# Performance work log

Measured on AMD Instinct MI355X. Metric: run time of the kernel, lower is better.

## Reference

```python
import jax, jax.numpy as jnp
import numpy as np

B, N = 16384, 20
F = 128          # n_node_features = n_neighbors_features = embed_dim
T = 100          # time_dim
E = 128          # n_edge_features
H = 2            # n_head
OUT = 128        # output_dimension
KEY_DIM = F + T + E  # 356


def setup_inputs() -> dict:
    key = jax.random.key(0)
    ks = jax.random.split(key, 24)
    s = 0.02
    inp = {
        "src_node_features": jax.random.normal(ks[0], (B, F), jnp.float32),
        "neighbors_features": jax.random.normal(ks[1], (B, N, F), jnp.float32),
        "neighbors_time_features": jax.random.normal(ks[2], (B, N, T), jnp.float32),
        "edge_features": jax.random.normal(ks[3], (B, N, E), jnp.float32),
        "neighbors_padding_mask": jax.random.randint(ks[4], (B, N), 0, 2).astype(bool),
        "weights": jax.random.uniform(ks[5], (B, N), jnp.float32),
        # transform: Linear(key_dim -> F)
        "Wt": jax.random.normal(ks[6], (F, KEY_DIM), jnp.float32) * s,
        "bt": jnp.zeros((F,), jnp.float32),
        # MultiheadAttention projections (embed_dim = kdim = vdim = F)
        "Wq": jax.random.normal(ks[7], (F, F), jnp.float32) * s,
        "bq": jnp.zeros((F,), jnp.float32),
        "Wk": jax.random.normal(ks[8], (F, F), jnp.float32) * s,
        "bk": jnp.zeros((F,), jnp.float32),
        "Wv": jax.random.normal(ks[9], (F, F), jnp.float32) * s,
        "bv": jnp.zeros((F,), jnp.float32),
        "Wo": jax.random.normal(ks[10], (F, F), jnp.float32) * s,
        "bo": jnp.zeros((F,), jnp.float32),
        # MergeLayer: fc1(query_dim + F -> F), fc2(F -> OUT)
        "W1": jax.random.normal(ks[11], (F, F + F), jnp.float32) * s,
        "b1": jnp.zeros((F,), jnp.float32),
        "W2": jax.random.normal(ks[12], (OUT, F), jnp.float32) * s,
        "b2": jnp.zeros((OUT,), jnp.float32),
    }
    return inp


def _gat_forward(src, nbr, timef, edgef, w, mask,
                 Wt, bt, Wq, bq, Wk, bk, Wv, bv, Wo, bo, W1, b1, W2, b2):
    b, f = src.shape
    dh = f // H
    scale = 1.0 / jnp.sqrt(jnp.asarray(dh, src.dtype))
    # key = transform(cat([nbr, edge, time])) * weights  -> [B,N,F]
    k_in = jnp.concatenate([nbr, edgef, timef], axis=2)
    keyv = (jnp.einsum('bnk,fk->bnf', k_in, Wt) + bt) * w[:, :, None]
    # invalid-neighborhood fixup: rows fully padded get their first slot unmasked
    invalid = mask.all(axis=1, keepdims=True)           # [B,1]
    mask = mask.at[:, 0].set(jnp.where(invalid[:, 0], False, mask[:, 0]))
    # projections (query_len = 1)
    q = (src @ Wq.T + bq).reshape(b, H, dh)             # [B,H,dh]
    k = (keyv @ Wk.T + bk).reshape(b, N, H, dh)         # [B,N,H,dh]
    v = (keyv @ Wv.T + bv).reshape(b, N, H, dh)
    scores = jnp.einsum('bhd,bnhd->bhn', q, k) * scale  # [B,H,N]
    scores = jnp.where(mask[:, None, :], -jnp.inf, scores)
    attn = jax.nn.softmax(scores, axis=-1)
    ctx = jnp.einsum('bhn,bnhd->bhd', attn, v).reshape(b, f)
    out = ctx @ Wo.T + bo                               # [B,F]
    out = jnp.where(invalid, jnp.asarray(0.0, out.dtype), out)
    out = jax.nn.relu(out)
    # MergeLayer: fc2(relu(fc1(cat([attn_out, src]))))
    hmid = jax.nn.relu(jnp.concatenate([out, src], axis=1) @ W1.T + b1)
    return hmid @ W2.T + b2


def reference(src_node_features, neighbors_features, neighbors_time_features,
              edge_features, neighbors_padding_mask, weights,
              Wt, bt, Wq, bq, Wk, bk, Wv, bv, Wo, bo, W1, b1, W2, b2):
    return _gat_forward(src_node_features, neighbors_features,
                        neighbors_time_features, edge_features, weights,
                        neighbors_padding_mask,
                        Wt, bt, Wq, bq, Wk, bk, Wv, bv, Wo, bo, W1, b1, W2, b2)
```

## Files before the change

kernel.cpp:

```cpp
#include <hip/hip_runtime.h>
#include <math.h>

#define NN 20
#define FF 128
#define TT 100
#define EE 128
#define KD 356

typedef unsigned int u32;
typedef unsigned short u16;
typedef unsigned long long u64;
typedef __attribute__((ext_vector_type(4))) float f32x4;
typedef __attribute__((ext_vector_type(8))) short s16x8;

__device__ __forceinline__ u16 f2b(float f) {
    u32 u = __float_as_uint(f);
    u32 r = u + 0x7FFFu + ((u >> 16) & 1u);
    return (u16)(r >> 16);
}
__device__ __forceinline__ float b2f(u16 h) { return __uint_as_float(((u32)h) << 16); }
__device__ __forceinline__ float blo(u32 u){ return __uint_as_float(u << 16); }
__device__ __forceinline__ float bhi(u32 u){ return __uint_as_float(u & 0xFFFF0000u); }
__device__ __forceinline__ u32 pk2(float a, float b){ return (u32)f2b(a) | ((u32)f2b(b) << 16); }


__global__ void prep_fuse(const float* __restrict__ Wt, const float* __restrict__ bt,
                          const float* __restrict__ Wk, const float* __restrict__ Wv,
                          const u32* __restrict__ maskw,
                          float* __restrict__ wkt, float* __restrict__ wvt,
                          float* __restrict__ kfb, float* __restrict__ vfb, int* __restrict__ flagp)
{
    const int blk = blockIdx.x, t = threadIdx.x;
    if (blk < KD) {
        __shared__ float col[FF];
        col[t] = Wt[t * KD + blk];
        __syncthreads();
        float ak = 0.f, av = 0.f;
        for (int j = 0; j < FF; ++j) {
            float c = col[j];
            ak = fmaf(Wk[t * FF + j], c, ak);
            av = fmaf(Wv[t * FF + j], c, av);
        }
        wkt[blk * FF + t] = ak;
        wvt[blk * FF + t] = av;
    } else if (blk == KD) {
        float ak = 0.f, av = 0.f;
        for (int j = 0; j < FF; ++j) {
            float c = bt[j];
            ak = fmaf(Wk[t * FF + j], c, ak);
            av = fmaf(Wv[t * FF + j], c, av);
        }
        kfb[t] = ak; vfb[t] = av;
    } else {
        int any = 0;
        for (int i = t; i < 8192; i += 128) any |= (maskw[i] > 1u) ? 1 : 0;
        any = __any(any) ? 1 : 0;
        __shared__ int red[2];
        if ((t & 63) == 0) red[t >> 6] = any;
        __syncthreads();
        if (t == 0) *flagp = (red[0] | red[1]) ? 1 : 0;
    }
}

__global__ void prep_pack_v3(const float* __restrict__ wkt, const float* __restrict__ wvt,
                             const float* __restrict__ Wq, const float* __restrict__ Wo,
                             const float* __restrict__ W1, const float* __restrict__ W2,
                             u16* __restrict__ kvB, u16* __restrict__ wqI, u16* __restrict__ woI,
                             u16* __restrict__ w1I, u16* __restrict__ w2I)
{
    const int id = blockIdx.x * 256 + threadIdx.x;
    if (id < 122880) {
        int kt = id / 10240, rem = id % 10240;
        int n = rem / 40, kk = rem % 40;
        int k = kt * 32 + kk;
        float v = 0.f;
        if (kk < 32 && k < KD) v = (n < FF) ? wkt[k * FF + n] : wvt[k * FF + (n - FF)];
        kvB[id] = f2b(v);
    } else if (id < 141312) {
        int e = id - 122880; int rem = e % 9216;
        int n = rem / 72, kk = rem % 72; int k = (e / 9216) * 64 + kk;
        wqI[e] = f2b(kk < 64 ? Wq[n * FF + k] : 0.f);
    } else if (id < 159744) {
        int e = id - 141312; int rem = e % 9216;
        int n = rem / 72, kk = rem % 72; int k = (e / 9216) * 64 + kk;
        woI[e] = f2b(kk < 64 ? Wo[n * FF + k] : 0.f);
    } else if (id < 196608) {
        int e = id - 159744; int rem = e % 9216;
        int n = rem / 72, kk = rem % 72; int k = (e / 9216) * 64 + kk;
        w1I[e] = f2b(kk < 64 ? W1[n * 2 * FF + k] : 0.f);
    } else if (id < 215040) {
        int e = id - 196608; int rem = e % 9216;
        int n = rem / 72, kk = rem % 72; int k = (e / 9216) * 64 + kk;
        w2I[e] = f2b(kk < 64 ? W2[n * FF + k] : 0.f);
    }
}

__device__ __forceinline__ void load_a_tile(const float* __restrict__ nbr,
                                            const float* __restrict__ edg,
                                            const float* __restrict__ tmf,
                                            size_t r, int cg, int kt, f32x4& v0, f32x4& v1)
{
    int c0 = cg * 8;
    if (kt < 4) {
        const float* p = nbr + r * 128 + kt * 32 + c0;
        v0 = *(const f32x4*)p; v1 = *(const f32x4*)(p + 4);
    } else if (kt < 8) {
        const float* p = edg + r * 128 + (kt - 4) * 32 + c0;
        v0 = *(const f32x4*)p; v1 = *(const f32x4*)(p + 4);
    } else {
        int c = (kt - 8) * 32 + c0;
        const float* p = tmf + r * 100 + c;
        v0 = (c + 3 < 100) ? *(const f32x4*)p : (f32x4){0.f,0.f,0.f,0.f};
        v1 = (c + 7 < 100) ? *(const f32x4*)(p + 4) : (f32x4){0.f,0.f,0.f,0.f};
    }
}

__global__ __launch_bounds__(512) void kv_gemm_v3(
    const float* __restrict__ nbr, const float* __restrict__ edg, const float* __restrict__ tmf,
    const float* __restrict__ wgt, const float* __restrict__ bk, const float* __restrict__ bv,
    const u16* __restrict__ kvB, const float* __restrict__ kfb, const float* __restrict__ vfb,
    u16* __restrict__ kvout)
{
    __shared__ u16 lA[128 * 40];
    __shared__ u16 lB[256 * 40];
    const int tid = threadIdx.x;
    const int Mbase = blockIdx.x * 128;
    const int lane = tid & 63, wave = tid >> 6;
    const int wm = wave >> 2, wn = wave & 3;
    const int row = tid >> 2;
    const int cg  = tid & 3;

    f32x4 acc[4][4] = {};
    const size_t r = (size_t)(Mbase + row);

    f32x4 v0, v1;
    load_a_tile(nbr, edg, tmf, r, cg, 0, v0, v1);

    for (int kt = 0; kt < 12; ++kt) {
        u32 p0 = pk2(v0.x, v0.y), p1 = pk2(v0.z, v0.w);
        u32 p2 = pk2(v1.x, v1.y), p3 = pk2(v1.z, v1.w);
        __syncthreads();
        *(uint4*)(&lA[row * 40 + cg * 8]) = make_uint4(p0, p1, p2, p3);
        for (int c = wave; c < 20; c += 8) {
            const char* g = (const char*)kvB + (size_t)kt * 20480 + c * 1024 + lane * 16;
            char* l = (char*)lB + c * 1024;
            __builtin_amdgcn_global_load_lds((const __attribute__((address_space(1))) u32*)g,
                                             (__attribute__((address_space(3))) u32*)l, 16, 0, 0);
        }
        if (kt < 11) load_a_tile(nbr, edg, tmf, r, cg, kt + 1, v0, v1);
        __syncthreads();

        const int kkb = (lane >> 4) * 8;
        s16x8 a[4], b[4];
        #pragma unroll
        for (int mt = 0; mt < 4; ++mt) {
            int m = wm * 64 + mt * 16 + (lane & 15);
            a[mt] = *(const s16x8*)(&lA[m * 40 + kkb]);
        }
        #pragma unroll
        for (int nt = 0; nt < 4; ++nt) {
            int n = wn * 64 + nt * 16 + (lane & 15);
            b[nt] = *(const s16x8*)(&lB[n * 40 + kkb]);
        }
        #pragma unroll
        for (int mt = 0; mt < 4; ++mt)
            #pragma unroll
            for (int nt = 0; nt < 4; ++nt)
                acc[mt][nt] = __builtin_amdgcn_mfma_f32_16x16x32_bf16(a[mt], b[nt], acc[mt][nt], 0, 0, 0);
    }

    #pragma unroll
    for (int mt = 0; mt < 4; ++mt) {
        float w4[4];
        #pragma unroll
        for (int i = 0; i < 4; ++i)
            w4[i] = wgt[Mbase + wm * 64 + mt * 16 + (lane >> 4) * 4 + i];
        #pragma unroll
        for (int nt = 0; nt < 4; ++nt) {
            int c = wn * 64 + nt * 16 + (lane & 15);
            float fb   = (c < FF) ? kfb[c] : vfb[c - FF];
            float bias = (c < FF) ? bk[c]  : bv[c - FF];
            #pragma unroll
            for (int i = 0; i < 4; ++i) {
                int rr = Mbase + wm * 64 + mt * 16 + (lane >> 4) * 4 + i;
                float val = fmaf(acc[mt][nt][i] + fb, w4[i], bias);
                kvout[(size_t)rr * 256 + c] = f2b(val);
            }
        }
    }
}

__global__ __launch_bounds__(64) void attn_lite(
    const u16* __restrict__ kv, const u16* __restrict__ Q, const void* __restrict__ maskp,
    const int* __restrict__ flagp, u16* __restrict__ ctx, unsigned char* __restrict__ flags)
{
    const int b = blockIdx.x, t = threadIdx.x;
    __shared__ u32 kls[NN][69];
    __shared__ float s_q[FF];
    __shared__ float s_sc[2 * NN];

    const int flag = *flagp;
    bool mybit = false;
    if (t < NN) {
        if (flag) mybit = ((const unsigned char*)maskp)[b * NN + t] != 0;
        else      mybit = ((const int*)maskp)[b * NN + t] != 0;
    }
    u64 bal = __ballot(mybit);
    u32 mb = (u32)(bal & 0xFFFFFull);
    const bool invalid = (mb == 0xFFFFFu);
    if (invalid) mb &= ~1u;
    if (t == 0) flags[b] = invalid ? 1 : 0;

    u32 qw = ((const u32*)Q)[(size_t)b * 64 + t];
    s_q[2 * t] = blo(qw); s_q[2 * t + 1] = bhi(qw);

    u32 vw[NN];
    const u32* kvp = (const u32*)kv + (size_t)b * NN * 128;
    #pragma unroll
    for (int n = 0; n < NN; ++n) {
        kls[n][t] = kvp[n * 128 + t];
        vw[n] = kvp[n * 128 + 64 + t];
    }
    __syncthreads();

    if (t < 2 * NN) {
        int h = t / NN, n = t - (t / NN) * NN;
        const u32* kr = &kls[n][h * 32];
        const float* qr = s_q + h * 64;
        float s = 0.f;
        #pragma unroll
        for (int d = 0; d < 32; ++d) {
            u32 u = kr[d];
            s = fmaf(qr[2 * d],     blo(u), s);
            s = fmaf(qr[2 * d + 1], bhi(u), s);
        }
        s *= 0.125f;
        s_sc[t] = ((mb >> n) & 1u) ? -INFINITY : s;
    }
    __syncthreads();
    if (t < 2) {
        float mx = -INFINITY;
        for (int n = 0; n < NN; ++n) mx = fmaxf(mx, s_sc[t * NN + n]);
        float e[NN]; float sum = 0.f;
        for (int n = 0; n < NN; ++n) { e[n] = expf(s_sc[t * NN + n] - mx); sum += e[n]; }
        float inv = 1.f / sum;
        for (int n = 0; n < NN; ++n) s_sc[t * NN + n] = e[n] * inv;
    }
    __syncthreads();

    const int h = t >> 5;
    float c0 = 0.f, c1 = 0.f;
    #pragma unroll
    for (int n = 0; n < NN; ++n) {
        float p = s_sc[h * NN + n];
        c0 = fmaf(p, blo(vw[n]), c0);
        c1 = fmaf(p, bhi(vw[n]), c1);
    }
    ((u32*)ctx)[(size_t)b * 64 + t] = pk2(c0, c1);
}

#define GM_Q 0
#define GM_O 1
#define GM_H 2
#define GM_F 3

template<int MODE>
__global__ __launch_bounds__(256) void gemm_small(
    const void* __restrict__ Asrc, const float* __restrict__ Asrc2,
    const u16* __restrict__ Bimg, const float* __restrict__ bias,
    const unsigned char* __restrict__ flags, void* __restrict__ outp)
{
    __shared__ u16 lA[64 * 72];
    __shared__ u16 lB[128 * 72];
    const int tid = threadIdx.x;
    const int Mbase = blockIdx.x * 64;
    const int lane = tid & 63, wave = tid >> 6;
    const int wm = wave >> 1, wn = wave & 1;
    const int row = tid >> 2, cg = tid & 3;

    constexpr int KTILES = (MODE == GM_H) ? 4 : 2;
    f32x4 acc[2][4] = {};
    const size_t r = (size_t)(Mbase + row);

    for (int kt = 0; kt < KTILES; ++kt) {
        if (MODE == GM_Q || (MODE == GM_H && kt >= 2)) {
            const float* ap = (MODE == GM_Q)
                ? ((const float*)Asrc + r * 128 + kt * 64 + cg * 16)
                : (Asrc2 + r * 128 + (kt - 2) * 64 + cg * 16);
            f32x4 x0 = *(const f32x4*)ap,       x1 = *(const f32x4*)(ap + 4);
            f32x4 x2 = *(const f32x4*)(ap + 8), x3 = *(const f32x4*)(ap + 12);
            *(uint4*)(&lA[row * 72 + cg * 16])     = make_uint4(pk2(x0.x,x0.y), pk2(x0.z,x0.w), pk2(x1.x,x1.y), pk2(x1.z,x1.w));
            *(uint4*)(&lA[row * 72 + cg * 16 + 8]) = make_uint4(pk2(x2.x,x2.y), pk2(x2.z,x2.w), pk2(x3.x,x3.y), pk2(x3.z,x3.w));
        } else {
            const u16* ap = (const u16*)Asrc + r * 128 + kt * 64 + cg * 16;
            *(uint4*)(&lA[row * 72 + cg * 16])     = *(const uint4*)ap;
            *(uint4*)(&lA[row * 72 + cg * 16 + 8]) = *(const uint4*)(ap + 8);
        }
        for (int c = wave; c < 18; c += 4) {
            const char* g = (const char*)Bimg + (size_t)kt * 18432 + c * 1024 + lane * 16;
            char* l = (char*)lB + c * 1024;
            __builtin_amdgcn_global_load_lds((const __attribute__((address_space(1))) u32*)g,
                                             (__attribute__((address_space(3))) u32*)l, 16, 0, 0);
        }
        __syncthreads();
        #pragma unroll
        for (int ks = 0; ks < 2; ++ks) {
            int kk = ks * 32 + (lane >> 4) * 8;
            s16x8 a[2], b[4];
            #pragma unroll
            for (int mt = 0; mt < 2; ++mt)
                a[mt] = *(const s16x8*)(&lA[(wm * 32 + mt * 16 + (lane & 15)) * 72 + kk]);
            #pragma unroll
            for (int nt = 0; nt < 4; ++nt)
                b[nt] = *(const s16x8*)(&lB[(wn * 64 + nt * 16 + (lane & 15)) * 72 + kk]);
            #pragma unroll
            for (int mt = 0; mt < 2; ++mt)
                #pragma unroll
                for (int nt = 0; nt < 4; ++nt)
                    acc[mt][nt] = __builtin_amdgcn_mfma_f32_16x16x32_bf16(a[mt], b[nt], acc[mt][nt], 0, 0, 0);
        }
        __syncthreads();
    }

    #pragma unroll
    for (int mt = 0; mt < 2; ++mt) {
        #pragma unroll
        for (int nt = 0; nt < 4; ++nt) {
            int colg = wn * 64 + nt * 16 + (lane & 15);
            float bb = bias[colg];
            #pragma unroll
            for (int i = 0; i < 4; ++i) {
                int rg = Mbase + wm * 32 + mt * 16 + (lane >> 4) * 4 + i;
                float val = acc[mt][nt][i] + bb;
                if (MODE == GM_O) { if (flags[rg]) val = 0.f; val = fmaxf(val, 0.f); }
                if (MODE == GM_H) val = fmaxf(val, 0.f);
                if (MODE == GM_F) ((float*)outp)[(size_t)rg * 128 + colg] = val;
                else              ((u16*)outp)[(size_t)rg * 128 + colg] = f2b(val);
            }
        }
    }
}


__global__ void prep_pack_r2(const float* __restrict__ wkt, const float* __restrict__ wvt,
                             const float* __restrict__ Wq, const float* __restrict__ Wo,
                             const float* __restrict__ W1, const float* __restrict__ W2,
                             u16* __restrict__ bpack, u32* __restrict__ wq2, u32* __restrict__ wo2,
                             u32* __restrict__ w12, u32* __restrict__ w22)
{
    const int id = blockIdx.x * 256 + threadIdx.x;
    if (id < 98304) {
        int kt = id >> 14;
        int o  = id & 16383;
        int n  = o >> 6;
        int kk = (o & 63) ^ ((n & 7) << 3);
        int k  = kt * 64 + kk;
        float v = 0.f;
        if (k < KD) v = (n < FF) ? wkt[k * FF + n] : wvt[k * FF + (n - FF)];
        bpack[id] = f2b(v);
    } else if (id < 106496) {
        int e = id - 98304; int j = e >> 6, tt = e & 63;
        wq2[e] = (u32)f2b(Wq[tt * FF + j]) | ((u32)f2b(Wq[(tt + 64) * FF + j]) << 16);
    } else if (id < 114688) {
        int e = id - 106496; int j = e >> 6, tt = e & 63;
        wo2[e] = (u32)f2b(Wo[tt * FF + j]) | ((u32)f2b(Wo[(tt + 64) * FF + j]) << 16);
    } else if (id < 131072) {
        int e = id - 114688; int j = e >> 6, tt = e & 63;
        w12[e] = (u32)f2b(W1[tt * 2 * FF + j]) | ((u32)f2b(W1[(tt + 64) * 2 * FF + j]) << 16);
    } else if (id < 139264) {
        int e = id - 131072; int j = e >> 6, tt = e & 63;
        w22[e] = (u32)f2b(W2[tt * FF + j]) | ((u32)f2b(W2[(tt + 64) * FF + j]) << 16);
    }
}

__global__ __launch_bounds__(512) void kv_gemm_r2(
    const float* __restrict__ nbr, const float* __restrict__ edg, const float* __restrict__ tmf,
    const float* __restrict__ wgt, const float* __restrict__ bk, const float* __restrict__ bv,
    const u16* __restrict__ bpack, const float* __restrict__ kfb, const float* __restrict__ vfb,
    u16* __restrict__ kvout)
{
    __shared__ u16 lA[128 * 64];
    __shared__ u16 lB[256 * 64];
    const int tid = threadIdx.x;
    const int Mbase = blockIdx.x * 128;
    const int lane = tid & 63, wave = tid >> 6;
    const int wm = wave >> 2, wn = wave & 3;

    f32x4 acc[4][4] = {};
    const int rq = tid >> 4;
    const int cq = tid & 15;

    for (int kt = 0; kt < 6; ++kt) {
        #pragma unroll
        for (int i = 0; i < 4; ++i) {
            int row = rq + i * 32;
            size_t r = (size_t)(Mbase + row);
            f32x4 v;
            if (kt < 2)       v = *(const f32x4*)(nbr + r * 128 + kt * 64 + cq * 4);
            else if (kt < 4)  v = *(const f32x4*)(edg + r * 128 + (kt - 2) * 64 + cq * 4);
            else if (kt == 4) v = *(const f32x4*)(tmf + r * 100 + cq * 4);
            else if (cq < 9)  v = *(const f32x4*)(tmf + r * 100 + 64 + cq * 4);
            else              v = (f32x4){0.f, 0.f, 0.f, 0.f};
            int off = row * 64 + ((cq * 4) ^ ((row & 7) << 3));
            *(uint2*)(&lA[off]) = make_uint2(pk2(v.x, v.y), pk2(v.z, v.w));
        }
        #pragma unroll
        for (int i = 0; i < 4; ++i) {
            int boff = wave * 4096 + i * 1024;
            const char* g = (const char*)bpack + (size_t)kt * 32768 + boff + lane * 16;
            char* l = (char*)lB + boff;
            __builtin_amdgcn_global_load_lds((const __attribute__((address_space(1))) u32*)g,
                                             (__attribute__((address_space(3))) u32*)l, 16, 0, 0);
        }
        __syncthreads();
        #pragma unroll
        for (int ks = 0; ks < 2; ++ks) {
            int kk = ks * 32 + (lane >> 4) * 8;
            s16x8 a[4], b[4];
            #pragma unroll
            for (int mt = 0; mt < 4; ++mt) {
                int m = wm * 64 + mt * 16 + (lane & 15);
                a[mt] = *(const s16x8*)(&lA[m * 64 + (kk ^ ((m & 7) << 3))]);
            }
            #pragma unroll
            for (int nt = 0; nt < 4; ++nt) {
                int n = wn * 64 + nt * 16 + (lane & 15);
                b[nt] = *(const s16x8*)(&lB[n * 64 + (kk ^ ((n & 7) << 3))]);
            }
            #pragma unroll
            for (int mt = 0; mt < 4; ++mt)
                #pragma unroll
                for (int nt = 0; nt < 4; ++nt)
                    acc[mt][nt] = __builtin_amdgcn_mfma_f32_16x16x32_bf16(a[mt], b[nt], acc[mt][nt], 0, 0, 0);
        }
        __syncthreads();
    }

    #pragma unroll
    for (int mt = 0; mt < 4; ++mt) {
        float w4[4];
        #pragma unroll
        for (int i = 0; i < 4; ++i)
            w4[i] = wgt[Mbase + wm * 64 + mt * 16 + (lane >> 4) * 4 + i];
        #pragma unroll
        for (int nt = 0; nt < 4; ++nt) {
            int c = wn * 64 + nt * 16 + (lane & 15);
            float fb   = (c < FF) ? kfb[c] : vfb[c - FF];
            float bias = (c < FF) ? bk[c]  : bv[c - FF];
            #pragma unroll
            for (int i = 0; i < 4; ++i) {
                int rr = Mbase + wm * 64 + mt * 16 + (lane >> 4) * 4 + i;
                float val = fmaf(acc[mt][nt][i] + fb, w4[i], bias);
                kvout[(size_t)rr * 256 + c] = f2b(val);
            }
        }
    }
}

__global__ __launch_bounds__(64) void gat_attn_r2(
    const float* __restrict__ src, const void* __restrict__ maskp,
    const float* __restrict__ bq, const float* __restrict__ bo,
    const float* __restrict__ b1, const float* __restrict__ b2,
    const u16* __restrict__ kv, const u32* __restrict__ wq2, const u32* __restrict__ wo2,
    const u32* __restrict__ w12, const u32* __restrict__ w22,
    const int* __restrict__ flagp, float* __restrict__ out)
{
    const int b = blockIdx.x, t = threadIdx.x;
    __shared__ u16 kls[NN * 132];
    __shared__ float s_src[FF], s_q[FF], s_ctx[FF], s_out[FF], s_h[FF];
    __shared__ float s_sc[2 * NN];

    const int flag = *flagp;
    bool mybit = false;
    if (t < NN) {
        if (flag) mybit = ((const unsigned char*)maskp)[b * NN + t] != 0;
        else      mybit = ((const int*)maskp)[b * NN + t] != 0;
    }
    u64 bal = __ballot(mybit);
    u32 mb = (u32)(bal & 0xFFFFFull);
    const bool invalid = (mb == 0xFFFFFu);
    if (invalid) mb &= ~1u;

    s_src[t] = src[(size_t)b * FF + t];
    s_src[t + 64] = src[(size_t)b * FF + 64 + t];

    float v0[NN], v1[NN];
    #pragma unroll
    for (int n = 0; n < NN; ++n) {
        const u16* row = kv + ((size_t)b * NN + n) * 256;
        kls[n * 132 + t]      = row[t];
        kls[n * 132 + 64 + t] = row[64 + t];
        v0[n] = b2f(row[128 + t]);
        v1[n] = b2f(row[192 + t]);
    }
    __syncthreads();

    {
        float q0 = bq[t], q1 = bq[64 + t];
        for (int j = 0; j < FF; ++j) {
            u32 u = wq2[j * 64 + t];
            float sj = s_src[j];
            q0 = fmaf(blo(u), sj, q0);
            q1 = fmaf(bhi(u), sj, q1);
        }
        s_q[t] = q0; s_q[64 + t] = q1;
    }
    __syncthreads();

    if (t < 2 * NN) {
        int h = t / NN, n = t - (t / NN) * NN;
        const u16* kr = kls + n * 132 + h * 64;
        const float* qr = s_q + h * 64;
        float s = 0.f;
        #pragma unroll
        for (int d = 0; d < 64; ++d) s = fmaf(qr[d], b2f(kr[d]), s);
        s *= 0.125f;
        s_sc[t] = ((mb >> n) & 1u) ? -INFINITY : s;
    }
    __syncthreads();
    if (t < 2) {
        float mx = -INFINITY;
        for (int n = 0; n < NN; ++n) mx = fmaxf(mx, s_sc[t * NN + n]);
        float e[NN]; float sum = 0.f;
        for (int n = 0; n < NN; ++n) { e[n] = expf(s_sc[t * NN + n] - mx); sum += e[n]; }
        float inv = 1.f / sum;
        for (int n = 0; n < NN; ++n) s_sc[t * NN + n] = e[n] * inv;
    }
    __syncthreads();

    {
        float c0 = 0.f, c1 = 0.f;
        #pragma unroll
        for (int n = 0; n < NN; ++n) {
            c0 = fmaf(s_sc[n],      v0[n], c0);
            c1 = fmaf(s_sc[NN + n], v1[n], c1);
        }
        s_ctx[t] = c0; s_ctx[64 + t] = c1;
    }
    __syncthreads();

    {
        float o0 = bo[t], o1 = bo[64 + t];
        for (int j = 0; j < FF; ++j) {
            u32 u = wo2[j * 64 + t];
            float cj = s_ctx[j];
            o0 = fmaf(blo(u), cj, o0);
            o1 = fmaf(bhi(u), cj, o1);
        }
        if (invalid) { o0 = 0.f; o1 = 0.f; }
        o0 = fmaxf(o0, 0.f); o1 = fmaxf(o1, 0.f);
        s_out[t] = o0; s_out[64 + t] = o1;
    }
    __syncthreads();

    {
        float h0 = b1[t], h1 = b1[64 + t];
        for (int j = 0; j < FF; ++j) {
            u32 u = w12[j * 64 + t];
            float xj = s_out[j];
            h0 = fmaf(blo(u), xj, h0);
            h1 = fmaf(bhi(u), xj, h1);
        }
        for (int j = 0; j < FF; ++j) {
            u32 u = w12[(FF + j) * 64 + t];
            float xj = s_src[j];
            h0 = fmaf(blo(u), xj, h0);
            h1 = fmaf(bhi(u), xj, h1);
        }
        h0 = fmaxf(h0, 0.f); h1 = fmaxf(h1, 0.f);
        s_h[t] = h0; s_h[64 + t] = h1;
    }
    __syncthreads();

    {
        float f0 = b2[t], f1 = b2[64 + t];
        for (int j = 0; j < FF; ++j) {
            u32 u = w22[j * 64 + t];
            float hj = s_h[j];
            f0 = fmaf(blo(u), hj, f0);
            f1 = fmaf(bhi(u), hj, f1);
        }
        out[(size_t)b * FF + t] = f0;
        out[(size_t)b * FF + 64 + t] = f1;
    }
}


#define FB_WKT  0
#define FB_WVT  (FB_WKT + KD*FF)
#define FB_KB   (FB_WVT + KD*FF)
#define FB_VB   (FB_KB + FF)
#define FB_WQT  (FB_VB + FF)
#define FB_WOT  (FB_WQT + FF*FF)
#define FB_W1T  (FB_WOT + FF*FF)
#define FB_W2T  (FB_W1T + 2*FF*FF)
#define FB_FLAG (FB_W2T + FF*FF)

__global__ void gat_prep_fb(const float* __restrict__ Wt, const float* __restrict__ bt,
                            const float* __restrict__ Wq, const float* __restrict__ Wk,
                            const float* __restrict__ Wv, const float* __restrict__ Wo,
                            const float* __restrict__ W1, const float* __restrict__ W2,
                            const u32* __restrict__ maskw, float* __restrict__ ws)
{
    const int blk = blockIdx.x;
    const int t = threadIdx.x;
    if (blk < KD) {
        __shared__ float col[FF];
        col[t] = Wt[t * KD + blk];
        __syncthreads();
        float ak = 0.f, av = 0.f;
        for (int j = 0; j < FF; ++j) {
            float c = col[j];
            ak = fmaf(Wk[t * FF + j], c, ak);
            av = fmaf(Wv[t * FF + j], c, av);
        }
        ws[FB_WKT + blk * FF + t] = ak;
        ws[FB_WVT + blk * FF + t] = av;
    } else if (blk == KD) {
        float ak = 0.f, av = 0.f;
        for (int j = 0; j < FF; ++j) {
            float c = bt[j];
            ak = fmaf(Wk[t * FF + j], c, ak);
            av = fmaf(Wv[t * FF + j], c, av);
        }
        ws[FB_KB + t] = ak;
        ws[FB_VB + t] = av;
    } else if (blk == KD + 1) {
        int any = 0;
        for (int i = t; i < 8192; i += 128) any |= (maskw[i] > 1u) ? 1 : 0;
        any = __any(any) ? 1 : 0;
        __shared__ int red[2];
        if ((t & 63) == 0) red[t >> 6] = any;
        __syncthreads();
        if (t == 0) ((int*)ws)[FB_FLAG] = (red[0] | red[1]) ? 1 : 0;
    } else {
        int id = (blk - (KD + 2)) * 128 + t;
        if (id < FF * FF) {
            int k = id >> 7, f = id & 127;
            ws[FB_WQT + id] = Wq[f * FF + k];
        } else if (id < 2 * FF * FF) {
            int e = id - FF * FF; int k = e >> 7, f = e & 127;
            ws[FB_WOT + e] = Wo[f * FF + k];
        } else if (id < 4 * FF * FF) {
            int e = id - 2 * FF * FF; int j = e >> 7, f = e & 127;
            ws[FB_W1T + e] = W1[f * (2 * FF) + j];
        } else if (id < 5 * FF * FF) {
            int e = id - 4 * FF * FF; int k = e >> 7, f = e & 127;
            ws[FB_W2T + e] = W2[f * FF + k];
        }
    }
}

__global__ __launch_bounds__(64) void gat_main_fb(
    const float* __restrict__ src, const float* __restrict__ nbr,
    const float* __restrict__ tmf, const float* __restrict__ edg,
    const void* __restrict__ maskp, const float* __restrict__ wgt,
    const float* __restrict__ bq, const float* __restrict__ bk,
    const float* __restrict__ bv, const float* __restrict__ bo,
    const float* __restrict__ b1, const float* __restrict__ b2,
    const float* __restrict__ ws, float* __restrict__ out)
{
    const int b = blockIdx.x;
    const int t = threadIdx.x;
    __shared__ __align__(16) float kin[KD * NN];
    __shared__ float s_src[FF], s_q[FF], s_ctx[FF], s_out[FF], s_h[FF];
    __shared__ float s_w[NN], s_sc[2 * NN];

    const int flag = ((const int*)ws)[FB_FLAG];
    bool mybit = false;
    if (t < NN) {
        if (flag) mybit = ((const unsigned char*)maskp)[b * NN + t] != 0;
        else      mybit = ((const int*)maskp)[b * NN + t] != 0;
    }
    u64 bal = __ballot(mybit);
    u32 mb = (u32)(bal & 0xFFFFFull);
    const bool invalid = (mb == 0xFFFFFu);
    if (invalid) mb &= ~1u;

    s_src[t] = src[(size_t)b * FF + t];
    s_src[t + 64] = src[(size_t)b * FF + 64 + t];
    if (t < NN) s_w[t] = wgt[(size_t)b * NN + t];

    for (int idx = t; idx < NN * FF; idx += 64) {
        int n = idx >> 7, j = idx & 127;
        kin[j * NN + n]         = nbr[((size_t)b * NN + n) * FF + j];
        kin[(128 + j) * NN + n] = edg[((size_t)b * NN + n) * EE + j];
    }
    for (int idx = t; idx < NN * TT; idx += 64) {
        int n = idx / TT, j = idx - n * TT;
        kin[(256 + j) * NN + n] = tmf[((size_t)b * NN + n) * TT + j];
    }
    __syncthreads();

    const float* wkt = ws + FB_WKT;
    const float* wvt = ws + FB_WVT;
    float ak0[NN], ak1[NN], av0[NN], av1[NN];
#pragma unroll
    for (int n = 0; n < NN; ++n) { ak0[n] = 0.f; ak1[n] = 0.f; av0[n] = 0.f; av1[n] = 0.f; }
    for (int k = 0; k < KD; ++k) {
        float wk0 = wkt[k * FF + t],      wk1 = wkt[k * FF + 64 + t];
        float wv0 = wvt[k * FF + t],      wv1 = wvt[k * FF + 64 + t];
        const float4* cp = (const float4*)(kin + k * NN);
        float4 ca = cp[0], cb = cp[1], cc = cp[2], cd = cp[3], ce = cp[4];
        const float c[NN] = { ca.x, ca.y, ca.z, ca.w,  cb.x, cb.y, cb.z, cb.w,
                              cc.x, cc.y, cc.z, cc.w,  cd.x, cd.y, cd.z, cd.w,
                              ce.x, ce.y, ce.z, ce.w };
#pragma unroll
        for (int n = 0; n < NN; ++n) {
            ak0[n] = fmaf(wk0, c[n], ak0[n]);
            ak1[n] = fmaf(wk1, c[n], ak1[n]);
            av0[n] = fmaf(wv0, c[n], av0[n]);
            av1[n] = fmaf(wv1, c[n], av1[n]);
        }
    }
    __syncthreads();

    float* kls = kin;
    float* vls = kin + NN * 129;
    {
        const float kb0 = ws[FB_KB + t], kb1 = ws[FB_KB + 64 + t];
        const float vb0 = ws[FB_VB + t], vb1 = ws[FB_VB + 64 + t];
        const float k0b = bk[t], k1b = bk[64 + t];
        const float v0b = bv[t], v1b = bv[64 + t];
#pragma unroll
        for (int n = 0; n < NN; ++n) {
            float wn = s_w[n];
            kls[n * 129 + t]      = fmaf(wn, ak0[n] + kb0, k0b);
            kls[n * 129 + 64 + t] = fmaf(wn, ak1[n] + kb1, k1b);
            vls[n * 129 + t]      = fmaf(wn, av0[n] + vb0, v0b);
            vls[n * 129 + 64 + t] = fmaf(wn, av1[n] + vb1, v1b);
        }
    }
    {
        const float* wqT = ws + FB_WQT;
        float q0 = bq[t], q1 = bq[64 + t];
        for (int j = 0; j < FF; ++j) {
            float sj = s_src[j];
            q0 = fmaf(wqT[j * FF + t], sj, q0);
            q1 = fmaf(wqT[j * FF + 64 + t], sj, q1);
        }
        s_q[t] = q0; s_q[64 + t] = q1;
    }
    __syncthreads();

    if (t < 2 * NN) {
        int h = t / NN, n = t - (t / NN) * NN;
        const float* kr = kls + n * 129 + h * 64;
        const float* qr = s_q + h * 64;
        float s = 0.f;
#pragma unroll
        for (int d = 0; d < 64; ++d) s = fmaf(qr[d], kr[d], s);
        s *= 0.125f;
        s_sc[t] = ((mb >> n) & 1u) ? -INFINITY : s;
    }
    __syncthreads();
    if (t < 2) {
        float mx = -INFINITY;
        for (int n = 0; n < NN; ++n) mx = fmaxf(mx, s_sc[t * NN + n]);
        float e[NN]; float sum = 0.f;
        for (int n = 0; n < NN; ++n) { e[n] = expf(s_sc[t * NN + n] - mx); sum += e[n]; }
        float inv = 1.f / sum;
        for (int n = 0; n < NN; ++n) s_sc[t * NN + n] = e[n] * inv;
    }
    __syncthreads();

    {
        float c0 = 0.f, c1 = 0.f;
#pragma unroll
        for (int n = 0; n < NN; ++n) {
            c0 = fmaf(s_sc[n],      vls[n * 129 + t],      c0);
            c1 = fmaf(s_sc[NN + n], vls[n * 129 + 64 + t], c1);
        }
        s_ctx[t] = c0; s_ctx[64 + t] = c1;
    }
    __syncthreads();

    {
        const float* woT = ws + FB_WOT;
        float o0 = bo[t], o1 = bo[64 + t];
        for (int j = 0; j < FF; ++j) {
            float cj = s_ctx[j];
            o0 = fmaf(woT[j * FF + t], cj, o0);
            o1 = fmaf(woT[j * FF + 64 + t], cj, o1);
        }
        if (invalid) { o0 = 0.f; o1 = 0.f; }
        o0 = fmaxf(o0, 0.f); o1 = fmaxf(o1, 0.f);
        s_out[t] = o0; s_out[64 + t] = o1;
    }
    __syncthreads();

    {
        const float* w1T = ws + FB_W1T;
        float h0 = b1[t], h1 = b1[64 + t];
        for (int j = 0; j < FF; ++j) {
            float xj = s_out[j];
            h0 = fmaf(w1T[j * FF + t], xj, h0);
            h1 = fmaf(w1T[j * FF + 64 + t], xj, h1);
        }
        for (int j = 0; j < FF; ++j) {
            float xj = s_src[j];
            h0 = fmaf(w1T[(FF + j) * FF + t], xj, h0);
            h1 = fmaf(w1T[(FF + j) * FF + 64 + t], xj, h1);
        }
        h0 = fmaxf(h0, 0.f); h1 = fmaxf(h1, 0.f);
        s_h[t] = h0; s_h[64 + t] = h1;
    }
    __syncthreads();

    {
        const float* w2T = ws + FB_W2T;
        float f0 = b2[t], f1 = b2[64 + t];
        for (int j = 0; j < FF; ++j) {
            float hj = s_h[j];
            f0 = fmaf(w2T[j * FF + t], hj, f0);
            f1 = fmaf(w2T[j * FF + 64 + t], hj, f1);
        }
        out[(size_t)b * FF + t] = f0;
        out[(size_t)b * FF + 64 + t] = f1;
    }
}


extern "C" void kernel_launch(void* const* d_in, const int* in_sizes, int n_in,
                              void* d_out, int out_size, void* d_ws, size_t ws_size,
                              hipStream_t stream)
{
    const float* src = (const float*)d_in[0];
    const float* nbr = (const float*)d_in[1];
    const float* tmf = (const float*)d_in[2];
    const float* edg = (const float*)d_in[3];
    const void*  msk = d_in[4];
    const float* wgt = (const float*)d_in[5];
    const float* Wt  = (const float*)d_in[6];
    const float* bt  = (const float*)d_in[7];
    const float* Wq  = (const float*)d_in[8];
    const float* bq  = (const float*)d_in[9];
    const float* Wk  = (const float*)d_in[10];
    const float* bk  = (const float*)d_in[11];
    const float* Wv  = (const float*)d_in[12];
    const float* bv  = (const float*)d_in[13];
    const float* Wo  = (const float*)d_in[14];
    const float* bo  = (const float*)d_in[15];
    const float* W1  = (const float*)d_in[16];
    const float* b1  = (const float*)d_in[17];
    const float* W2  = (const float*)d_in[18];
    const float* b2  = (const float*)d_in[19];

    const int B = in_sizes[0] / FF;
    const size_t M = (size_t)B * NN;

    size_t o1 = 0;
    size_t t1_kv   = o1; o1 += M * 512;
    size_t t1_qa   = o1; o1 += (size_t)B * 256;
    size_t t1_ch   = o1; o1 += (size_t)B * 256;
    size_t t1_kvB  = o1; o1 += 245760;
    size_t t1_wqI  = o1; o1 += 36864;
    size_t t1_woI  = o1; o1 += 36864;
    size_t t1_w1I  = o1; o1 += 73728;
    size_t t1_w2I  = o1; o1 += 36864;
    size_t t1_wkt  = o1; o1 += (size_t)KD * FF * 4;
    size_t t1_wvt  = o1; o1 += (size_t)KD * FF * 4;
    size_t t1_kfb  = o1; o1 += 512;
    size_t t1_vfb  = o1; o1 += 512;
    size_t t1_flg  = o1; o1 += (size_t)B;
    o1 = (o1 + 255) & ~(size_t)255;
    size_t t1_flag = o1; o1 += 64;
    const size_t need1 = o1;

    size_t o2 = 0;
    size_t t2_kv    = o2; o2 += M * 512;
    size_t t2_bpack = o2; o2 += 98304ull * 2;
    size_t t2_wkt   = o2; o2 += (size_t)KD * FF * 4;
    size_t t2_wvt   = o2; o2 += (size_t)KD * FF * 4;
    size_t t2_kfb   = o2; o2 += 512;
    size_t t2_vfb   = o2; o2 += 512;
    size_t t2_wq2   = o2; o2 += 32768;
    size_t t2_wo2   = o2; o2 += 32768;
    size_t t2_w12   = o2; o2 += 65536;
    size_t t2_w22   = o2; o2 += 32768;
    size_t t2_flag  = o2; o2 += 64;
    const size_t need2 = o2;

    char* w = (char*)d_ws;

    if (ws_size >= need1 && (M % 128) == 0 && (B % 64) == 0) {
        u16*   kvp   = (u16*)(w + t1_kv);
        u16*   qa    = (u16*)(w + t1_qa);
        u16*   ch    = (u16*)(w + t1_ch);
        u16*   kvB   = (u16*)(w + t1_kvB);
        u16*   wqI   = (u16*)(w + t1_wqI);
        u16*   woI   = (u16*)(w + t1_woI);
        u16*   w1I   = (u16*)(w + t1_w1I);
        u16*   w2I   = (u16*)(w + t1_w2I);
        float* wktp  = (float*)(w + t1_wkt);
        float* wvtp  = (float*)(w + t1_wvt);
        float* kfb   = (float*)(w + t1_kfb);
        float* vfb   = (float*)(w + t1_vfb);
        unsigned char* flg = (unsigned char*)(w + t1_flg);
        int*   flagp = (int*)(w + t1_flag);

        prep_fuse<<<dim3(KD + 2), dim3(128), 0, stream>>>(Wt, bt, Wk, Wv,
            (const u32*)msk, wktp, wvtp, kfb, vfb, flagp);
        prep_pack_v3<<<dim3(840), dim3(256), 0, stream>>>(wktp, wvtp, Wq, Wo, W1, W2,
            kvB, wqI, woI, w1I, w2I);
        kv_gemm_v3<<<dim3((int)(M / 128)), dim3(512), 0, stream>>>(
            nbr, edg, tmf, wgt, bk, bv, kvB, kfb, vfb, kvp);
        gemm_small<GM_Q><<<dim3(B / 64), dim3(256), 0, stream>>>(
            (const void*)src, nullptr, wqI, bq, nullptr, (void*)qa);
        attn_lite<<<dim3(B), dim3(64), 0, stream>>>(kvp, qa, msk, flagp, ch, flg);
        gemm_small<GM_O><<<dim3(B / 64), dim3(256), 0, stream>>>(
            (const void*)ch, nullptr, woI, bo, flg, (void*)qa);
        gemm_small<GM_H><<<dim3(B / 64), dim3(256), 0, stream>>>(
            (const void*)qa, src, w1I, b1, nullptr, (void*)ch);
        gemm_small<GM_F><<<dim3(B / 64), dim3(256), 0, stream>>>(
            (const void*)ch, nullptr, w2I, b2, nullptr, d_out);
    } else if (ws_size >= need2 && (M % 128) == 0) {
        u16*   kvp   = (u16*)(w + t2_kv);
        u16*   bpack = (u16*)(w + t2_bpack);
        float* wktp  = (float*)(w + t2_wkt);
        float* wvtp  = (float*)(w + t2_wvt);
        float* kfb   = (float*)(w + t2_kfb);
        float* vfb   = (float*)(w + t2_vfb);
        u32*   wq2   = (u32*)(w + t2_wq2);
        u32*   wo2   = (u32*)(w + t2_wo2);
        u32*   w12   = (u32*)(w + t2_w12);
        u32*   w22   = (u32*)(w + t2_w22);
        int*   flagp = (int*)(w + t2_flag);

        prep_fuse<<<dim3(KD + 2), dim3(128), 0, stream>>>(Wt, bt, Wk, Wv,
            (const u32*)msk, wktp, wvtp, kfb, vfb, flagp);
        prep_pack_r2<<<dim3(544), dim3(256), 0, stream>>>(wktp, wvtp, Wq, Wo, W1, W2,
            bpack, wq2, wo2, w12, w22);
        kv_gemm_r2<<<dim3((int)(M / 128)), dim3(512), 0, stream>>>(
            nbr, edg, tmf, wgt, bk, bv, bpack, kfb, vfb, kvp);
        gat_attn_r2<<<dim3(B), dim3(64), 0, stream>>>(
            src, msk, bq, bo, b1, b2, kvp, wq2, wo2, w12, w22, flagp, (float*)d_out);
    } else {
        float* ws = (float*)d_ws;
        gat_prep_fb<<<dim3(KD + 2 + 640), dim3(128), 0, stream>>>(
            Wt, bt, Wq, Wk, Wv, Wo, W1, W2, (const u32*)msk, ws);
        gat_main_fb<<<dim3(B), dim3(64), 0, stream>>>(
            src, nbr, tmf, edg, msk, wgt, bq, bk, bv, bo, b1, b2, ws, (float*)d_out);
    }
}
```

Baseline: 239.0 us.

## Fuse KV projection GEMM with attention per 8-node tile, double-buffer LDS

Merges the K/V projection GEMM and the attention kernel into one kernel. Each block handles 8 batch rows (160 neighbor rows), stages the bf16 K/V results in LDS and computes scores, softmax and context there. This removes the global round trip of the M×256 bf16 KV intermediate and one launch. The GEMM main loop also gains double-buffered A/B tiles with a swizzled A layout so loads overlap the MFMAs. The cost is more LDS per block and a two-phase epilogue with extra syncs, which may lower occupancy.

```diff
diff --git a/kernel.cpp b/kernel.cpp
--- a/kernel.cpp
+++ b/kernel.cpp
@@ -6,6 +6,7 @@
 #define TT 100
 #define EE 128
 #define KD 356
+#define BM 160
 
 typedef unsigned int u32;
 typedef unsigned short u16;
@@ -95,12 +96,12 @@
     }
 }
 
-__device__ __forceinline__ void load_a_tile(const float* __restrict__ nbr,
-                                            const float* __restrict__ edg,
-                                            const float* __restrict__ tmf,
-                                            size_t r, int cg, int kt, f32x4& v0, f32x4& v1)
-{
-    int c0 = cg * 8;
+__device__ __forceinline__ void loadA32(const float* __restrict__ nbr,
+                                        const float* __restrict__ edg,
+                                        const float* __restrict__ tmf,
+                                        size_t r, int g, int kt, f32x4& v0, f32x4& v1)
+{
+    int c0 = g * 8;
     if (kt < 4) {
         const float* p = nbr + r * 128 + kt * 32 + c0;
         v0 = *(const f32x4*)p; v1 = *(const f32x4*)(p + 4);
@@ -110,153 +111,166 @@
     } else {
         int c = (kt - 8) * 32 + c0;
         const float* p = tmf + r * 100 + c;
-        v0 = (c + 3 < 100) ? *(const f32x4*)p : (f32x4){0.f,0.f,0.f,0.f};
+        v0 = (c + 3 < 100) ? *(const f32x4*)p       : (f32x4){0.f,0.f,0.f,0.f};
         v1 = (c + 7 < 100) ? *(const f32x4*)(p + 4) : (f32x4){0.f,0.f,0.f,0.f};
     }
 }
 
-__global__ __launch_bounds__(512) void kv_gemm_v3(
+__device__ __forceinline__ void writeA(u16* __restrict__ lA, int row, int g,
+                                       const f32x4& v0, const f32x4& v1)
+{
+    int off = ((row >> 4) * 4 + g) * 128 + (row & 15) * 8;
+    *(uint4*)(&lA[off]) = make_uint4(pk2(v0.x,v0.y), pk2(v0.z,v0.w), pk2(v1.x,v1.y), pk2(v1.z,v1.w));
+}
+
+__global__ __launch_bounds__(512) void kv_attn_fused(
     const float* __restrict__ nbr, const float* __restrict__ edg, const float* __restrict__ tmf,
     const float* __restrict__ wgt, const float* __restrict__ bk, const float* __restrict__ bv,
     const u16* __restrict__ kvB, const float* __restrict__ kfb, const float* __restrict__ vfb,
-    u16* __restrict__ kvout)
-{
-    __shared__ u16 lA[128 * 40];
-    __shared__ u16 lB[256 * 40];
-    const int tid = threadIdx.x;
-    const int Mbase = blockIdx.x * 128;
+    const u16* __restrict__ Qg, const void* __restrict__ maskp, const int* __restrict__ flagp,
+    u16* __restrict__ ctxout, unsigned char* __restrict__ flags)
+{
+    __shared__ __align__(16) u16 smem[2*5120 + 2*10240];
+    u16* kvls = smem;
+
+    const int tid  = threadIdx.x;
     const int lane = tid & 63, wave = tid >> 6;
     const int wm = wave >> 2, wn = wave & 3;
-    const int row = tid >> 2;
-    const int cg  = tid & 3;
-
-    f32x4 acc[4][4] = {};
-    const size_t r = (size_t)(Mbase + row);
-
-    f32x4 v0, v1;
-    load_a_tile(nbr, edg, tmf, r, cg, 0, v0, v1);
-
+    const int Bbase = blockIdx.x * 8;
+    const int Mbase = blockIdx.x * BM;
+
+    const int srow = tid >> 2;
+    const int sg   = tid & 3;
+    const bool has2 = (tid < 128);
+    const int srow2 = 128 + (tid >> 2);
+
+    f32x4 acc[5][4] = {};
+    f32x4 a0, a1, c0v, c1v;
+
+    loadA32(nbr, edg, tmf, (size_t)(Mbase + srow), sg, 0, a0, a1);
+    if (has2) loadA32(nbr, edg, tmf, (size_t)(Mbase + srow2), sg, 0, c0v, c1v);
+    writeA(smem, srow, sg, a0, a1);
+    if (has2) writeA(smem, srow2, sg, c0v, c1v);
+    for (int c = wave; c < 20; c += 8) {
+        const char* g = (const char*)kvB + c * 1024 + lane * 16;
+        char* l = (char*)(smem + 2*5120) + c * 1024;
+        __builtin_amdgcn_global_load_lds((const __attribute__((address_space(1))) u32*)g,
+                                         (__attribute__((address_space(3))) u32*)l, 16, 0, 0);
+    }
+    __syncthreads();
+
+    int cur = 0;
     for (int kt = 0; kt < 12; ++kt) {
-        u32 p0 = pk2(v0.x, v0.y), p1 = pk2(v0.z, v0.w);
-        u32 p2 = pk2(v1.x, v1.y), p3 = pk2(v1.z, v1.w);
+        u16* curA = smem + cur * 5120;
+        u16* curB = smem + 2*5120 + cur * 10240;
+        u16* nxtA = smem + (cur ^ 1) * 5120;
+        u16* nxtB = smem + 2*5120 + (cur ^ 1) * 10240;
+
+        if (kt < 11) {
+            loadA32(nbr, edg, tmf, (size_t)(Mbase + srow), sg, kt + 1, a0, a1);
+            if (has2) loadA32(nbr, edg, tmf, (size_t)(Mbase + srow2), sg, kt + 1, c0v, c1v);
+            for (int c = wave; c < 20; c += 8) {
+                const char* g = (const char*)kvB + (size_t)(kt + 1) * 20480 + c * 1024 + lane * 16;
+                char* l = (char*)nxtB + c * 1024;
+                __builtin_amdgcn_global_load_lds((const __attribute__((address_space(1))) u32*)g,
+                                                 (__attribute__((address_space(3))) u32*)l, 16, 0, 0);
+            }
+        }
+
+        const int kg = lane >> 4, l16 = lane & 15;
+        s16x8 af[5], bf[4];
+        #pragma unroll
+        for (int mt = 0; mt < 5; ++mt)
+            af[mt] = *(const s16x8*)(&curA[((wm * 5 + mt) * 4 + kg) * 128 + l16 * 8]);
+        #pragma unroll
+        for (int nt = 0; nt < 4; ++nt)
+            bf[nt] = *(const s16x8*)(&curB[(wn * 64 + nt * 16 + l16) * 40 + kg * 8]);
+        #pragma unroll
+        for (int mt = 0; mt < 5; ++mt)
+            #pragma unroll
+            for (int nt = 0; nt < 4; ++nt)
+                acc[mt][nt] = __builtin_amdgcn_mfma_f32_16x16x32_bf16(af[mt], bf[nt], acc[mt][nt], 0, 0, 0);
+
+        if (kt < 11) {
+            writeA(nxtA, srow, sg, a0, a1);
+            if (has2) writeA(nxtA, srow2, sg, c0v, c1v);
+        }
         __syncthreads();
-        *(uint4*)(&lA[row * 40 + cg * 8]) = make_uint4(p0, p1, p2, p3);
-        for (int c = wave; c < 20; c += 8) {
-            const char* g = (const char*)kvB + (size_t)kt * 20480 + c * 1024 + lane * 16;
-            char* l = (char*)lB + c * 1024;
-            __builtin_amdgcn_global_load_lds((const __attribute__((address_space(1))) u32*)g,
-                                             (__attribute__((address_space(3))) u32*)l, 16, 0, 0);
-        }
-        if (kt < 11) load_a_tile(nbr, edg, tmf, r, cg, kt + 1, v0, v1);
+        cur ^= 1;
+    }
+
+    const int flagv = *flagp;
+    for (int ph = 0; ph < 2; ++ph) {
+        if (ph == 1) __syncthreads();
+        if (wm == ph) {
+            #pragma unroll
+            for (int mt = 0; mt < 5; ++mt) {
+                int r0 = mt * 16 + (lane >> 4) * 4;
+                float w4[4];
+                #pragma unroll
+                for (int i = 0; i < 4; ++i) w4[i] = wgt[Mbase + ph * 80 + r0 + i];
+                #pragma unroll
+                for (int nt = 0; nt < 4; ++nt) {
+                    int c = wn * 64 + nt * 16 + (lane & 15);
+                    float fb = (c < FF) ? kfb[c] : vfb[c - FF];
+                    float bb = (c < FF) ? bk[c]  : bv[c - FF];
+                    #pragma unroll
+                    for (int i = 0; i < 4; ++i)
+                        kvls[(r0 + i) * 264 + c] = f2b(fmaf(acc[mt][nt][i] + fb, w4[i], bb));
+                }
+            }
+        }
         __syncthreads();
 
-        const int kkb = (lane >> 4) * 8;
-        s16x8 a[4], b[4];
-        #pragma unroll
-        for (int mt = 0; mt < 4; ++mt) {
-            int m = wm * 64 + mt * 16 + (lane & 15);
-            a[mt] = *(const s16x8*)(&lA[m * 40 + kkb]);
-        }
-        #pragma unroll
-        for (int nt = 0; nt < 4; ++nt) {
-            int n = wn * 64 + nt * 16 + (lane & 15);
-            b[nt] = *(const s16x8*)(&lB[n * 40 + kkb]);
-        }
-        #pragma unroll
-        for (int mt = 0; mt < 4; ++mt)
-            #pragma unroll
-            for (int nt = 0; nt < 4; ++nt)
-                acc[mt][nt] = __builtin_amdgcn_mfma_f32_16x16x32_bf16(a[mt], b[nt], acc[mt][nt], 0, 0, 0);
-    }
-
-    #pragma unroll
-    for (int mt = 0; mt < 4; ++mt) {
-        float w4[4];
-        #pragma unroll
-        for (int i = 0; i < 4; ++i)
-            w4[i] = wgt[Mbase + wm * 64 + mt * 16 + (lane >> 4) * 4 + i];
-        #pragma unroll
-        for (int nt = 0; nt < 4; ++nt) {
-            int c = wn * 64 + nt * 16 + (lane & 15);
-            float fb   = (c < FF) ? kfb[c] : vfb[c - FF];
-            float bias = (c < FF) ? bk[c]  : bv[c - FF];
-            #pragma unroll
-            for (int i = 0; i < 4; ++i) {
-                int rr = Mbase + wm * 64 + mt * 16 + (lane >> 4) * 4 + i;
-                float val = fmaf(acc[mt][nt][i] + fb, w4[i], bias);
-                kvout[(size_t)rr * 256 + c] = f2b(val);
+        {
+            const int lb = wave >> 1, h = wave & 1;
+            const int brow = Bbase + ph * 4 + lb;
+            bool mybit = false;
+            if (lane < NN) {
+                if (flagv) mybit = ((const unsigned char*)maskp)[brow * NN + lane] != 0;
+                else       mybit = ((const int*)maskp)[brow * NN + lane] != 0;
             }
-        }
-    }
-}
-
-__global__ __launch_bounds__(64) void attn_lite(
-    const u16* __restrict__ kv, const u16* __restrict__ Q, const void* __restrict__ maskp,
-    const int* __restrict__ flagp, u16* __restrict__ ctx, unsigned char* __restrict__ flags)
-{
-    const int b = blockIdx.x, t = threadIdx.x;
-    __shared__ u32 kls[NN][69];
-    __shared__ float s_q[FF];
-    __shared__ float s_sc[2 * NN];
-
-    const int flag = *flagp;
-    bool mybit = false;
-    if (t < NN) {
-        if (flag) mybit = ((const unsigned char*)maskp)[b * NN + t] != 0;
-        else      mybit = ((const int*)maskp)[b * NN + t] != 0;
-    }
-    u64 bal = __ballot(mybit);
-    u32 mb = (u32)(bal & 0xFFFFFull);
-    const bool invalid = (mb == 0xFFFFFu);
-    if (invalid) mb &= ~1u;
-    if (t == 0) flags[b] = invalid ? 1 : 0;
-
-    u32 qw = ((const u32*)Q)[(size_t)b * 64 + t];
-    s_q[2 * t] = blo(qw); s_q[2 * t + 1] = bhi(qw);
-
-    u32 vw[NN];
-    const u32* kvp = (const u32*)kv + (size_t)b * NN * 128;
-    #pragma unroll
-    for (int n = 0; n < NN; ++n) {
-        kls[n][t] = kvp[n * 128 + t];
-        vw[n] = kvp[n * 128 + 64 + t];
-    }
-    __syncthreads();
-
-    if (t < 2 * NN) {
-        int h = t / NN, n = t - (t / NN) * NN;
-        const u32* kr = &kls[n][h * 32];
-        const float* qr = s_q + h * 64;
-        float s = 0.f;
-        #pragma unroll
-        for (int d = 0; d < 32; ++d) {
-            u32 u = kr[d];
-            s = fmaf(qr[2 * d],     blo(u), s);
-            s = fmaf(qr[2 * d + 1], bhi(u), s);
-        }
-        s *= 0.125f;
-        s_sc[t] = ((mb >> n) & 1u) ? -INFINITY : s;
-    }
-    __syncthreads();
-    if (t < 2) {
-        float mx = -INFINITY;
-        for (int n = 0; n < NN; ++n) mx = fmaxf(mx, s_sc[t * NN + n]);
-        float e[NN]; float sum = 0.f;
-        for (int n = 0; n < NN; ++n) { e[n] = expf(s_sc[t * NN + n] - mx); sum += e[n]; }
-        float inv = 1.f / sum;
-        for (int n = 0; n < NN; ++n) s_sc[t * NN + n] = e[n] * inv;
-    }
-    __syncthreads();
-
-    const int h = t >> 5;
-    float c0 = 0.f, c1 = 0.f;
-    #pragma unroll
-    for (int n = 0; n < NN; ++n) {
-        float p = s_sc[h * NN + n];
-        c0 = fmaf(p, blo(vw[n]), c0);
-        c1 = fmaf(p, bhi(vw[n]), c1);
-    }
-    ((u32*)ctx)[(size_t)b * 64 + t] = pk2(c0, c1);
+            u64 bal = __ballot(mybit);
+            u32 mb = (u32)(bal & 0xFFFFFull);
+            const bool invalid = (mb == 0xFFFFFu);
+            if (invalid) mb &= ~1u;
+            if (h == 0 && lane == 0) flags[brow] = invalid ? 1 : 0;
+
+            const int n = lane & 31;
+            float s = -INFINITY;
+            if (lane < 32 && n < NN) {
+                const u16* kr = &kvls[(lb * NN + n) * 264 + h * 64];
+                const u16* qr = Qg + (size_t)brow * 128 + h * 64;
+                float d = 0.f;
+                #pragma unroll
+                for (int dc = 0; dc < 8; ++dc) {
+                    uint4 kw = *(const uint4*)(kr + dc * 8);
+                    uint4 qw = *(const uint4*)(qr + dc * 8);
+                    d = fmaf(blo(kw.x), blo(qw.x), d);  d = fmaf(bhi(kw.x), bhi(qw.x), d);
+                    d = fmaf(blo(kw.y), blo(qw.y), d);  d = fmaf(bhi(kw.y), bhi(qw.y), d);
+                    d = fmaf(blo(kw.z), blo(qw.z), d);  d = fmaf(bhi(kw.z), bhi(qw.z), d);
+                    d = fmaf(blo(kw.w), blo(qw.w), d);  d = fmaf(bhi(kw.w), bhi(qw.w), d);
+                }
+                s = ((mb >> n) & 1u) ? -INFINITY : d * 0.125f;
+            }
+            float mx = s;
+            #pragma unroll
+            for (int off = 16; off; off >>= 1) mx = fmaxf(mx, __shfl_xor(mx, off, 32));
+            float e = (lane < 32 && n < NN) ? expf(s - mx) : 0.f;
+            float sum = e;
+            #pragma unroll
+            for (int off = 16; off; off >>= 1) sum += __shfl_xor(sum, off, 32);
+            float p = e / sum;
+
+            float cacc = 0.f;
+            #pragma unroll
+            for (int nn2 = 0; nn2 < NN; ++nn2) {
+                float pn = __shfl(p, nn2);
+                cacc = fmaf(pn, b2f(kvls[(lb * NN + nn2) * 264 + 128 + h * 64 + lane]), cacc);
+            }
+            ctxout[(size_t)brow * 128 + h * 64 + lane] = f2b(cacc);
+        }
+    }
 }
 
 #define GM_Q 0
@@ -850,7 +864,6 @@
     const size_t M = (size_t)B * NN;
 
     size_t o1 = 0;
-    size_t t1_kv   = o1; o1 += M * 512;
     size_t t1_qa   = o1; o1 += (size_t)B * 256;
     size_t t1_ch   = o1; o1 += (size_t)B * 256;
     size_t t1_kvB  = o1; o1 += 245760;
@@ -883,8 +896,7 @@
 
     char* w = (char*)d_ws;
 
-    if (ws_size >= need1 && (M % 128) == 0 && (B % 64) == 0) {
-        u16*   kvp   = (u16*)(w + t1_kv);
+    if (ws_size >= need1 && (B % 64) == 0) {
         u16*   qa    = (u16*)(w + t1_qa);
         u16*   ch    = (u16*)(w + t1_ch);
         u16*   kvB   = (u16*)(w + t1_kvB);
@@ -903,11 +915,10 @@
             (const u32*)msk, wktp, wvtp, kfb, vfb, flagp);
         prep_pack_v3<<<dim3(840), dim3(256), 0, stream>>>(wktp, wvtp, Wq, Wo, W1, W2,
             kvB, wqI, woI, w1I, w2I);
-        kv_gemm_v3<<<dim3((int)(M / 128)), dim3(512), 0, stream>>>(
-            nbr, edg, tmf, wgt, bk, bv, kvB, kfb, vfb, kvp);
         gemm_small<GM_Q><<<dim3(B / 64), dim3(256), 0, stream>>>(
             (const void*)src, nullptr, wqI, bq, nullptr, (void*)qa);
-        attn_lite<<<dim3(B), dim3(64), 0, stream>>>(kvp, qa, msk, flagp, ch, flg);
+        kv_attn_fused<<<dim3(B / 8), dim3(512), 0, stream>>>(
+            nbr, edg, tmf, wgt, bk, bv, kvB, kfb, vfb, qa, msk, flagp, ch, flg);
         gemm_small<GM_O><<<dim3(B / 64), dim3(256), 0, stream>>>(
             (const void*)ch, nullptr, woI, bo, flg, (void*)qa);
         gemm_small<GM_H><<<dim3(B / 64), dim3(256), 0, stream>>>(
```

Result: slower. 279.6 us (+17.0%).
